# Performance work log

Measured on AMD Instinct MI355X. Metric: run time of the kernel, lower is better.

## Reference

```python
import jax, jax.numpy as jnp
import numpy as np

B, L, DIM, H, D, WS = 2, 2048, 1024, 16, 64, 256
SCALE = D ** -0.5


def _rope_tables(seq_len, dim, dtype):
    inv_freq = 1.0 / (10000.0 ** (jnp.arange(0, dim, 2, dtype=jnp.float32) / dim))
    t = jnp.arange(seq_len, dtype=jnp.float32)
    freqs = jnp.einsum('i,j->ij', t, inv_freq)          # [L, D/2]
    emb = jnp.concatenate([freqs, freqs], axis=-1)       # [L, D]
    return jnp.cos(emb).astype(dtype), jnp.sin(emb).astype(dtype)


def _rotate_half(x):
    x1, x2 = x[..., : x.shape[-1] // 2], x[..., x.shape[-1] // 2:]
    return jnp.concatenate([-x2, x1], axis=-1)


def _apply_rope(t, cos, sin):
    # t: [B, L, H, D]; cos/sin: [L, D] broadcast over batch and heads
    return t * cos[None, :, None, :] + _rotate_half(t) * sin[None, :, None, :]


def setup_inputs() -> dict:
    key = jax.random.key(0)
    k0, k1, k2 = jax.random.split(key, 3)
    x = jax.random.normal(k0, (B, L, DIM), dtype=jnp.float32)
    Wqkv = jax.random.normal(k1, (3 * H * D, DIM), dtype=jnp.float32) * 0.02
    bqkv = jnp.zeros((3 * H * D,), dtype=jnp.float32)
    Wproj = jax.random.normal(k2, (DIM, H * D), dtype=jnp.float32) * 0.02
    bproj = jnp.zeros((DIM,), dtype=jnp.float32)
    return {"x": x, "Wqkv": Wqkv, "bqkv": bqkv, "Wproj": Wproj, "bproj": bproj, "is_global": 1}


def _attention(x, Wqkv, bqkv, Wproj, bproj, is_global):
    b, l, _ = x.shape
    qkv = x @ Wqkv.T + bqkv                              # [B, L, 3*H*D]
    q, k, v = jnp.split(qkv, 3, axis=-1)
    q, k, v = (t.reshape(b, l, H, D) for t in (q, k, v))
    cos, sin = _rope_tables(l, D, x.dtype)
    q = _apply_rope(q, cos, sin)
    k = _apply_rope(k, cos, sin)
    if is_global:
        attn = jnp.einsum('bshd,bthd->bhst', q, k) * SCALE
        attn = jax.nn.softmax(attn, axis=-1)
        out = jnp.einsum('bhst,bthd->bshd', attn, v)     # [B, L, H, D]
    else:
        pad = (WS - l % WS) % WS
        if pad > 0:
            q, k, v = (jnp.pad(t, ((0, 0), (0, pad), (0, 0), (0, 0))) for t in (q, k, v))
        w = (l + pad) // WS
        q = q.reshape(b, w, WS, H, D)
        k = k.reshape(b, w, WS, H, D)
        v = v.reshape(b, w, WS, H, D)
        attn = jnp.einsum('bwshd,bwthd->bwhst', q, k) * SCALE
        attn = jax.nn.softmax(attn, axis=-1)
        out = jnp.einsum('bwhst,bwthd->bwshd', attn, v).reshape(b, w * WS, H, D)
        out = out[:, :l]
    return out.reshape(b, l, H * D) @ Wproj.T + bproj


def reference(x, Wqkv, bqkv, Wproj, bproj, is_global):
    return _attention(x, Wqkv, bqkv, Wproj, bproj, is_global)
```

## Files before the change

### kernel.cpp

```cpp
#include <hip/hip_runtime.h>
#include <math.h>

#define NB 2
#define NL 2048
#define NDIM 1024
#define NH 16
#define ND 64
#define NWS 256
#define NM (NB*NL)
#define QSCALE 0.18033688011112042f

typedef __attribute__((ext_vector_type(8))) short short8;
typedef __attribute__((ext_vector_type(4))) float f32x4;
typedef unsigned short ushort_t;
typedef unsigned int uint_t;

#define MFMA16(a,b,acc) __builtin_amdgcn_mfma_f32_16x16x32_bf16((a),(b),(acc),0,0,0)

static __device__ __forceinline__ ushort_t f2bf(float x){
    uint_t u = __float_as_uint(x);
    uint_t r = (u + 0x7fff + ((u >> 16) & 1)) >> 16;
    return (ushort_t)r;
}
static __device__ __forceinline__ float bf2f(ushort_t u){
    return __uint_as_float(((uint_t)u) << 16);
}
static __device__ __forceinline__ float fast_exp2(float x){
#if __has_builtin(__builtin_amdgcn_exp2f)
    return __builtin_amdgcn_exp2f(x);
#else
    return exp2f(x);
#endif
}

static __device__ __forceinline__ void async_load16(const void* g, void* l){
    __builtin_amdgcn_global_load_lds(
        (const __attribute__((address_space(1))) unsigned int*)g,
        (__attribute__((address_space(3))) unsigned int*)l, 16, 0, 0);
}

__launch_bounds__(256)
__global__ void split_hl(const float* __restrict__ in, ushort_t* __restrict__ oh,
                         ushort_t* __restrict__ ol)
{
    const int i = (blockIdx.x*256 + threadIdx.x)*4;
    const float4 v = *(const float4*)(in + i);
    ushort_t h0=f2bf(v.x), h1=f2bf(v.y), h2=f2bf(v.z), h3=f2bf(v.w);
    ushort4 h4; h4.x=h0; h4.y=h1; h4.z=h2; h4.w=h3;
    ushort4 l4;
    l4.x=f2bf(v.x - bf2f(h0)); l4.y=f2bf(v.y - bf2f(h1));
    l4.z=f2bf(v.z - bf2f(h2)); l4.w=f2bf(v.w - bf2f(h3));
    *(ushort4*)(oh + i) = h4;
    *(ushort4*)(ol + i) = l4;
}

__launch_bounds__(256)
__global__ void rope_tab(float* __restrict__ tc, float* __restrict__ ts)
{
    const int idx = blockIdx.x*256 + threadIdx.x;
    const int j = idx >> 11, l = idx & (NL-1);
    const float invf = 1.0f / powf(10000.0f, (float)j * (1.0f/32.0f));
    float s, c;
    sincosf((float)l * invf, &s, &c);
    tc[idx] = c; ts[idx] = s;
}

template<int MODE>
__launch_bounds__(256, 4)
__global__ void gemm_hl(const ushort_t* __restrict__ Ah, const ushort_t* __restrict__ Al,
                        const ushort_t* __restrict__ Bh, const ushort_t* __restrict__ Bl,
                        const float* __restrict__ bias,
                        float* __restrict__ Cout,
                        ushort_t* __restrict__ oQh, ushort_t* __restrict__ oKh,
                        ushort_t* __restrict__ oVth,
                        const float* __restrict__ tcos, const float* __restrict__ tsin)
{
    __shared__ __align__(16) char smem[(MODE==0) ? 36864 : 32768];
    ushort_t* sA_h = (ushort_t*)smem;
    ushort_t* sA_l = (ushort_t*)(smem + 8192);
    ushort_t* sB_h = (ushort_t*)(smem + 16384);
    ushort_t* sB_l = (MODE==1) ? (ushort_t*)(smem + 24576) : sB_h;
    ushort_t* sBounce = (ushort_t*)smem;

    const int tid  = threadIdx.x;
    const int wv   = tid >> 6, lane = tid & 63;
    const int quad = lane >> 4, l16 = lane & 15;
    const int m0 = blockIdx.y << 7, n0 = blockIdx.x << 7;
    const int wr = wv >> 1, wc = wv & 1;

    const ushort_t* gsrc;
    ushort_t* lds_base;
    int rowb, npass;
    if (MODE == 1) {
        gsrc = (wv==0)?Ah:(wv==1)?Al:(wv==2)?Bh:Bl;
        lds_base = (wv==0)?sA_h:(wv==1)?sA_l:(wv==2)?sB_h:sB_l;
        rowb = (wv < 2) ? m0 : n0;
        npass = 8;
    } else {
        if (wv == 0)      { gsrc = Ah; lds_base = sA_h; rowb = m0; npass = 8; }
        else if (wv == 1) { gsrc = Al; lds_base = sA_l; rowb = m0; npass = 8; }
        else { gsrc = Bh; lds_base = sB_h + (wv-2)*64*32; rowb = n0 + (wv-2)*64; npass = 4; }
    }
    const int rl = lane >> 2;
    const int cp = lane & 3;
    const int cg = cp ^ ((rl >> 1) & 3);
    const ushort_t* gptr = gsrc + (size_t)(rowb + rl)*NDIM + cg*8;

    f32x4 acc[4][4];
    #pragma unroll
    for (int i=0;i<4;++i)
        #pragma unroll
        for (int j=0;j<4;++j) acc[i][j] = (f32x4){0.f,0.f,0.f,0.f};

    const int swz = (l16 >> 1) & 3;
    const int ac_off = (wr*64 + l16)*32 + ((quad ^ swz) << 3);
    const int bc_off = (wc*64 + l16)*32 + ((quad ^ swz) << 3);

    for (int k0 = 0; k0 < NDIM; k0 += 32) {
        __syncthreads();
        const ushort_t* gp = gptr + k0;
        for (int p=0; p<npass; ++p)
            async_load16(gp + (size_t)p*16*NDIM, (char*)lds_base + p*1024);
        __syncthreads();

        short8 ah[4], al[4], bh[4], bl[4];
        #pragma unroll
        for (int t=0;t<4;++t){
            ah[t] = *(const short8*)&sA_h[t*512 + ac_off];
            al[t] = *(const short8*)&sA_l[t*512 + ac_off];
            bh[t] = *(const short8*)&sB_h[t*512 + bc_off];
            if (MODE == 1) bl[t] = *(const short8*)&sB_l[t*512 + bc_off];
        }
        #pragma unroll
        for (int mt=0;mt<4;++mt)
            #pragma unroll
            for (int nt=0;nt<4;++nt){
                f32x4 a = acc[mt][nt];
                a = MFMA16(ah[mt], bh[nt], a);
                a = MFMA16(al[mt], bh[nt], a);
                if (MODE == 1) a = MFMA16(ah[mt], bl[nt], a);
                acc[mt][nt] = a;
            }
    }

    if (MODE == 1) {
        const int colb = n0 + wc*64;
        float bq[4];
        #pragma unroll
        for (int nt=0;nt<4;++nt) bq[nt] = bias[colb + nt*16 + l16];
        #pragma unroll
        for (int mt=0;mt<4;++mt)
            #pragma unroll
            for (int r=0;r<4;++r){
                const int m = m0 + wr*64 + mt*16 + quad*4 + r;
                float* orow = Cout + (size_t)m*NDIM + colb;
                #pragma unroll
                for (int nt=0;nt<4;++nt)
                    orow[nt*16 + l16] = acc[mt][nt][r] + bq[nt];
            }
    } else {
        const int colb = n0 + wc*64;
        const int sel  = colb >> 10;
        const int head = (colb & 1023) >> 6;
        float bq[4];
        #pragma unroll
        for (int nt=0;nt<4;++nt) bq[nt] = bias[colb + nt*16 + l16];

        if (sel == 2) {
            __syncthreads();
            const int bb = m0 >> 11;
            const int Lb = (m0 & (NL-1)) + wr*64;
            ushort_t* sT = sBounce + wv*(64*72);
            const size_t gb = ((size_t)(bb*NH + head)*ND)*NL + Lb;
            const int drow = lane >> 3, dcol = lane & 7;
            #pragma unroll
            for (int mt=0;mt<4;++mt)
                #pragma unroll
                for (int nt=0;nt<4;++nt)
                    #pragma unroll
                    for (int r=0;r<4;++r)
                        sT[(nt*16+l16)*72 + mt*16 + quad*4 + r] = f2bf(acc[mt][nt][r] + bq[nt]);
            #pragma unroll
            for (int dd=0; dd<8; ++dd){
                const int d = dd*8 + drow;
                const uint4 v = *(const uint4*)&sT[d*72 + dcol*8];
                *(uint4*)(oVth + gb + (size_t)d*NL + dcol*8) = v;
            }
        } else {
            ushort_t* dh = sel ? oKh : oQh;
            const float qs = sel ? 1.0f : QSCALE;
            #pragma unroll
            for (int mt=0;mt<4;++mt)
                #pragma unroll
                for (int r=0;r<4;++r){
                    const int m = m0 + wr*64 + mt*16 + quad*4 + r;
                    const int bb = m >> 11, l = m & (NL-1);
                    const size_t ro = ((size_t)((bb*NH + head)*NL + l)) << 6;
                    #pragma unroll
                    for (int ntp=0;ntp<2;++ntp){
                        const int j = ntp*16 + l16;
                        const float c = tcos[j*NL + l];
                        const float s = tsin[j*NL + l];
                        const float x1 = acc[mt][ntp  ][r] + bq[ntp];
                        const float x2 = acc[mt][ntp+2][r] + bq[ntp+2];
                        const int d1 = ntp*16 + l16;
                        dh[ro + d1]      = f2bf((x1*c - x2*s) * qs);
                        dh[ro + d1 + 32] = f2bf((x2*c + x1*s) * qs);
                    }
                }
        }
    }
}

__launch_bounds__(256, 4)
__global__ void attn_mfma(const ushort_t* __restrict__ Qh,
                          const ushort_t* __restrict__ Kh,
                          const ushort_t* __restrict__ Vth,
                          ushort_t* __restrict__ AOh, ushort_t* __restrict__ AOl,
                          const int* __restrict__ isg)
{
    __shared__ __align__(16) char smem[40960];

    const int tid  = threadIdx.x;
    const int wv   = tid >> 6, lane = tid & 63;
    const int quad = lane >> 4, l16 = lane & 15;
    const int bh = blockIdx.x & 31, qt = blockIdx.x >> 5;
    const int q0w = qt*64 + wv*16;

    short8 bq0, bq1;
    {
        const size_t rb = (((size_t)bh*NL + q0w) << 6) + (size_t)(l16 << 6) + quad*8;
        bq0 = *(const short8*)(Qh + rb);
        bq1 = *(const short8*)(Qh + rb + 32);
    }
    short8 ones;
    #pragma unroll
    for (int j=0;j<8;++j) ones[j] = (short)0x3F80;

    f32x4 o[4];
    #pragma unroll
    for (int dnt=0; dnt<4; ++dnt) o[dnt] = (f32x4){0.f,0.f,0.f,0.f};
    f32x4 lsacc = (f32x4){0.f,0.f,0.f,0.f};

    const int gflag = isg[0];
    int klo, khi;
    if (gflag) { klo = 0; khi = NL; }
    else       { klo = (qt >> 2)*NWS; khi = klo + NWS; }

    const int swz4 = (l16 & 7) << 4;
    const int KC0 = l16*128 + (( quad*16      ) ^ swz4);
    const int KC1 = l16*128 + (( quad*16 + 64 ) ^ swz4);
    const int sPb = 32768 + wv*2048;
    int PW[4];
    #pragma unroll
    for (int knt=0; knt<4; ++knt)
        PW[knt] = sPb + l16*128 + ((knt*32 + quad*8) ^ swz4);
    const int PR0 = sPb + KC0;
    const int PR1 = sPb + KC1;

    const int r8  = lane >> 3;
    const int c8s = (lane & 7) ^ r8;
    const ushort_t* Kp = Kh + (((size_t)bh*NL) << 6)
                       + (size_t)(klo + wv*16 + r8)*64 + c8s*8;
    const ushort_t* Vp = Vth + (size_t)bh*ND*NL
                       + (size_t)(wv*16 + r8)*NL + klo + c8s*8;
    const int kdst = wv*2048;
    const int vdst = 16384 + wv*2048;

#define STAGE(BUF) do { \
        async_load16(Kp,          smem + (BUF)*8192 + kdst); \
        async_load16(Kp + 512,    smem + (BUF)*8192 + kdst + 1024); \
        async_load16(Vp,          smem + (BUF)*8192 + vdst); \
        async_load16(Vp + 8*NL,   smem + (BUF)*8192 + vdst + 1024); \
        Kp += 64*64; Vp += 64; } while (0)

#define TILE(BUF) do { \
        const char* kb_ = smem + (BUF)*8192; \
        const char* vb_ = smem + 16384 + (BUF)*8192; \
        f32x4 s_[4]; \
        _Pragma("unroll") \
        for (int knt=0; knt<4; ++knt) { \
            const short8 a0 = *(const short8*)(kb_ + knt*2048 + KC0); \
            const short8 a1 = *(const short8*)(kb_ + knt*2048 + KC1); \
            f32x4 t = (f32x4){0.f,0.f,0.f,0.f}; \
            t = MFMA16(a0, bq0, t); \
            t = MFMA16(a1, bq1, t); \
            s_[knt] = t; \
        } \
        _Pragma("unroll") \
        for (int knt=0; knt<4; ++knt) { \
            const uint_t u0 = __float_as_uint(fast_exp2(s_[knt][0])); \
            const uint_t u1 = __float_as_uint(fast_exp2(s_[knt][1])); \
            const uint_t u2 = __float_as_uint(fast_exp2(s_[knt][2])); \
            const uint_t u3 = __float_as_uint(fast_exp2(s_[knt][3])); \
            uint2 pk_; \
            pk_.x = __builtin_amdgcn_perm(u1, u0, 0x07060302u); \
            pk_.y = __builtin_amdgcn_perm(u3, u2, 0x07060302u); \
            *(uint2*)(smem + PW[knt]) = pk_; \
        } \
        const short8 fp0 = *(const short8*)(smem + PR0); \
        const short8 fp1 = *(const short8*)(smem + PR1); \
        lsacc = MFMA16(fp0, ones, lsacc); \
        lsacc = MFMA16(fp1, ones, lsacc); \
        _Pragma("unroll") \
        for (int dnt=0; dnt<4; ++dnt) { \
            const short8 v0 = *(const short8*)(vb_ + dnt*2048 + KC0); \
            const short8 v1 = *(const short8*)(vb_ + dnt*2048 + KC1); \
            f32x4 t = o[dnt]; \
            t = MFMA16(fp0, v0, t); \
            t = MFMA16(fp1, v1, t); \
            o[dnt] = t; \
        } } while (0)

    STAGE(0);
    for (int kt = klo; kt < khi; kt += 128) {
        __syncthreads();
        if (kt + 64 < khi) STAGE(1);
        TILE(0);
        __syncthreads();
        if (kt + 128 < khi) STAGE(0);
        TILE(1);
    }
#undef STAGE
#undef TILE

    const int bb = bh >> 4, hh = bh & 15;
    #pragma unroll
    for (int r=0; r<4; ++r) {
        const float inv = 1.0f / lsacc[r];
        const int row = q0w + quad*4 + r;
        const size_t ob = (((size_t)(bb*NL + row)) << 10) + (hh << 6);
        #pragma unroll
        for (int dnt=0; dnt<4; ++dnt) {
            const float val = o[dnt][r] * inv;
            const ushort_t h = f2bf(val);
            AOh[ob + dnt*16 + l16] = h;
            AOl[ob + dnt*16 + l16] = f2bf(val - bf2f(h));
        }
    }
}

extern "C" void kernel_launch(void* const* d_in, const int* in_sizes, int n_in,
                              void* d_out, int out_size, void* d_ws, size_t ws_size,
                              hipStream_t stream)
{
    const float* x     = (const float*)d_in[0];
    const float* Wqkv  = (const float*)d_in[1];
    const float* bqkv  = (const float*)d_in[2];
    const float* Wproj = (const float*)d_in[3];
    const float* bproj = (const float*)d_in[4];
    const int*   isg   = (const int*)d_in[5];
    float* out = (float*)d_out;
    char* base = (char*)d_ws;

    const size_t MB = 1024*1024;
    ushort_t* Qh  = (ushort_t*)(base);
    ushort_t* Kh  = (ushort_t*)(base + 16*MB);
    ushort_t* Vth = (ushort_t*)(base + 32*MB);
    ushort_t* xh  = (ushort_t*)(base + 48*MB);
    ushort_t* xl  = (ushort_t*)(base + 56*MB);
    ushort_t* AOh = xh;
    ushort_t* AOl = xl;
    ushort_t* Wqh = (ushort_t*)(base + 64*MB);
    ushort_t* Wql = (ushort_t*)(base + 64*MB + 6291456);
    ushort_t* Wph = (ushort_t*)(base + 76*MB);
    ushort_t* Wpl = (ushort_t*)(base + 76*MB + 2097152);
    float*    tcs = (float*)(base + 80*MB);
    float*    tsn = (float*)(base + 80*MB + 262144);

    split_hl<<<4096, 256, 0, stream>>>(x, xh, xl);
    split_hl<<<3072, 256, 0, stream>>>(Wqkv, Wqh, Wql);
    split_hl<<<1024, 256, 0, stream>>>(Wproj, Wph, Wpl);
    rope_tab<<<256, 256, 0, stream>>>(tcs, tsn);

    gemm_hl<0><<<dim3(3*NDIM/128, NM/128), 256, 0, stream>>>(
        xh, xl, Wqh, Wql, bqkv, nullptr,
        Qh, Kh, Vth, tcs, tsn);

    attn_mfma<<<NB*NH*(NL/64), 256, 0, stream>>>(
        Qh, Kh, Vth, AOh, AOl, isg);

    gemm_hl<1><<<dim3(NDIM/128, NM/128), 256, 0, stream>>>(
        AOh, AOl, Wph, Wpl, bproj, out,
        nullptr, nullptr, nullptr, nullptr, nullptr);
}
```

Measured before the change: 241.7 us.

## Double-buffer LDS tiles in the QKV GEMM to overlap loads with MFMA

```diff
diff --git a/kernel.cpp b/kernel.cpp
--- a/kernel.cpp
+++ b/kernel.cpp
@@ -66,7 +66,7 @@
 }
 
 template<int MODE>
-__launch_bounds__(256, 4)
+__launch_bounds__(256, (MODE==0) ? 3 : 4)
 __global__ void gemm_hl(const ushort_t* __restrict__ Ah, const ushort_t* __restrict__ Al,
                         const ushort_t* __restrict__ Bh, const ushort_t* __restrict__ Bl,
                         const float* __restrict__ bias,
@@ -75,12 +75,14 @@
                         ushort_t* __restrict__ oVth,
                         const float* __restrict__ tcos, const float* __restrict__ tsin)
 {
-    __shared__ __align__(16) char smem[(MODE==0) ? 36864 : 32768];
+    __shared__ __align__(16) char smem[(MODE==0) ? 50176 : 32768];
     ushort_t* sA_h = (ushort_t*)smem;
     ushort_t* sA_l = (ushort_t*)(smem + 8192);
     ushort_t* sB_h = (ushort_t*)(smem + 16384);
     ushort_t* sB_l = (MODE==1) ? (ushort_t*)(smem + 24576) : sB_h;
     ushort_t* sBounce = (ushort_t*)smem;
+    const int ebuf = 12288;
+    const int bbuf = 24576;
 
     const int tid  = threadIdx.x;
     const int wv   = tid >> 6, lane = tid & 63;
@@ -116,32 +118,54 @@
     const int ac_off = (wr*64 + l16)*32 + ((quad ^ swz) << 3);
     const int bc_off = (wc*64 + l16)*32 + ((quad ^ swz) << 3);
 
-    for (int k0 = 0; k0 < NDIM; k0 += 32) {
-        __syncthreads();
-        const ushort_t* gp = gptr + k0;
-        for (int p=0; p<npass; ++p)
-            async_load16(gp + (size_t)p*16*NDIM, (char*)lds_base + p*1024);
-        __syncthreads();
-
-        short8 ah[4], al[4], bh[4], bl[4];
-        #pragma unroll
-        for (int t=0;t<4;++t){
-            ah[t] = *(const short8*)&sA_h[t*512 + ac_off];
-            al[t] = *(const short8*)&sA_l[t*512 + ac_off];
-            bh[t] = *(const short8*)&sB_h[t*512 + bc_off];
-            if (MODE == 1) bl[t] = *(const short8*)&sB_l[t*512 + bc_off];
+#define GSTAGE(BUF, KOFF) do { \
+        const ushort_t* gp_ = gptr + (KOFF); \
+        for (int p=0; p<npass; ++p) \
+            async_load16(gp_ + (size_t)p*16*NDIM, (char*)lds_base + (BUF)*bbuf + p*1024); \
+    } while(0)
+
+#define GCOMP(BUF) do { \
+        const int eo_ = (BUF)*ebuf; \
+        short8 ah[4], al[4], bh[4], bl[4]; \
+        _Pragma("unroll") \
+        for (int t=0;t<4;++t){ \
+            ah[t] = *(const short8*)&sA_h[eo_ + t*512 + ac_off]; \
+            al[t] = *(const short8*)&sA_l[eo_ + t*512 + ac_off]; \
+            bh[t] = *(const short8*)&sB_h[eo_ + t*512 + bc_off]; \
+            if (MODE == 1) bl[t] = *(const short8*)&sB_l[eo_ + t*512 + bc_off]; \
+        } \
+        _Pragma("unroll") \
+        for (int mt=0;mt<4;++mt) \
+            _Pragma("unroll") \
+            for (int nt=0;nt<4;++nt){ \
+                f32x4 a_ = acc[mt][nt]; \
+                a_ = MFMA16(ah[mt], bh[nt], a_); \
+                a_ = MFMA16(al[mt], bh[nt], a_); \
+                if (MODE == 1) a_ = MFMA16(ah[mt], bl[nt], a_); \
+                acc[mt][nt] = a_; \
+            } \
+    } while(0)
+
+    if (MODE == 0) {
+        GSTAGE(0, 0);
+        for (int k0 = 0; k0 < NDIM; k0 += 64) {
+            __syncthreads();
+            GSTAGE(1, k0 + 32);
+            GCOMP(0);
+            __syncthreads();
+            if (k0 + 64 < NDIM) GSTAGE(0, k0 + 64);
+            GCOMP(1);
         }
-        #pragma unroll
-        for (int mt=0;mt<4;++mt)
-            #pragma unroll
-            for (int nt=0;nt<4;++nt){
-                f32x4 a = acc[mt][nt];
-                a = MFMA16(ah[mt], bh[nt], a);
-                a = MFMA16(al[mt], bh[nt], a);
-                if (MODE == 1) a = MFMA16(ah[mt], bl[nt], a);
-                acc[mt][nt] = a;
-            }
-    }
+    } else {
+        for (int k0 = 0; k0 < NDIM; k0 += 32) {
+            __syncthreads();
+            GSTAGE(0, k0);
+            __syncthreads();
+            GCOMP(0);
+        }
+    }
+#undef GSTAGE
+#undef GCOMP
 
     if (MODE == 1) {
         const int colb = n0 + wc*64;
```

After: 232.6 us. 3.8% less time.
